# Optimization experiments

Measured on AMD Instinct MI355X. Metric: run time of the kernel, lower is better.

## Reference

```python
import jax, jax.numpy as jnp
import numpy as np

B, S, E = 4, 2048, 512
H = 8
DK = E // H          # 64
NQ = 8               # n_qubits


def setup_inputs() -> dict:
    key = jax.random.key(0)
    ks = jax.random.split(key, 10)
    s = 1.0 / np.sqrt(E)
    return {
        "x": jax.random.normal(ks[0], (B, S, E), dtype=jnp.float32),
        "Wq": jax.random.normal(ks[1], (E, E), dtype=jnp.float32) * s,
        "bq": jnp.zeros((E,), dtype=jnp.float32),
        "Wk": jax.random.normal(ks[2], (E, E), dtype=jnp.float32) * s,
        "bk": jnp.zeros((E,), dtype=jnp.float32),
        "Wv": jax.random.normal(ks[3], (E, E), dtype=jnp.float32) * s,
        "bv": jnp.zeros((E,), dtype=jnp.float32),
        "Wo": jax.random.normal(ks[4], (E, E), dtype=jnp.float32) * s,
        "bo": jnp.zeros((E,), dtype=jnp.float32),
        "kernel_params": jax.random.normal(ks[5], (NQ, NQ), dtype=jnp.float32),
    }


def _split_heads(t):
    # [B,S,E] -> [B,H,S,DK]
    return t.reshape(B, S, H, DK).transpose(0, 2, 1, 3)


def reference(x, Wq, bq, Wk, bk, Wv, bv, Wo, bo, kernel_params):
    q = _split_heads(x @ Wq + bq)
    k = _split_heads(x @ Wk + bk)
    v = _split_heads(x @ Wv + bv)

    # Quantum kernel closed form: RX(x_i) then RZ(theta_ii) on wire i, measure <Z_i>.
    # RZ commutes with Z so <Z_i> = cos(x_i). Only the first NQ features are encoded.
    q_meas = jnp.cos(q[..., :NQ])  # [B,H,S,NQ]
    k_meas = jnp.cos(k[..., :NQ])  # [B,H,S,NQ]

    sim = jnp.einsum('bhqd,bhkd->bhqk', q_meas, k_meas)  # [B,H,S,S]
    attn = jax.nn.softmax(sim, axis=-1)
    out = jnp.einsum('bhqk,bhkd->bhqd', attn, v)          # [B,H,S,DK]
    out = out.transpose(0, 2, 1, 3).reshape(B, S, E)      # compose heads
    return out @ Wo + bo
```

## Files before the change

### kernel.cpp

```cpp
#include <hip/hip_runtime.h>
#include <hip/hip_bf16.h>

#define BB 4
#define SS 2048
#define EE 512
#define HH 8
#define DKK 64
#define NQQ 8
#define BS (BB * SS)

typedef __attribute__((ext_vector_type(8))) short bf16x8;
typedef __attribute__((ext_vector_type(4))) float f32x4;
typedef __attribute__((ext_vector_type(16))) float f32x16;
typedef _Float16 f16x4 __attribute__((ext_vector_type(4)));
typedef _Float16 f16x8 __attribute__((ext_vector_type(8)));
typedef unsigned short u16;
typedef unsigned int u32;

union U2H { uint2 u; f16x4 h; };
union U4H8 { uint4 u; f16x8 h; };

__device__ __forceinline__ u16 f2bf(float f) {
    union { float f; u32 u; } v; v.f = f;
    u32 r = v.u + 0x7fffu + ((v.u >> 16) & 1u);
    return (u16)(r >> 16);
}
__device__ __forceinline__ float bf2f(u16 h) {
    union { u32 u; float f; } v; v.u = ((u32)h) << 16;
    return v.f;
}
__device__ __forceinline__ u16 f2h(float f) {
    _Float16 hv = (_Float16)f;
    return *reinterpret_cast<u16*>(&hv);
}

__global__ __launch_bounds__(256) void cvt2_kernel(
    const float4* __restrict__ in, uint2* __restrict__ xh, uint2* __restrict__ xl, int n4)
{
    int i = blockIdx.x * 256 + threadIdx.x;
    if (i >= n4) return;
    float4 a = in[i];
    u16 h0 = f2bf(a.x), h1 = f2bf(a.y), h2 = f2bf(a.z), h3 = f2bf(a.w);
    u16 l0 = f2bf(a.x - bf2f(h0)), l1 = f2bf(a.y - bf2f(h1));
    u16 l2 = f2bf(a.z - bf2f(h2)), l3 = f2bf(a.w - bf2f(h3));
    xh[i] = make_uint2((u32)h0 | ((u32)h1 << 16), (u32)h2 | ((u32)h3 << 16));
    xl[i] = make_uint2((u32)l0 | ((u32)l1 << 16), (u32)l2 | ((u32)l3 << 16));
}

__global__ __launch_bounds__(256) void wqk_pack_kernel(
    const float* __restrict__ Wq, const float* __restrict__ Wk,
    u16* __restrict__ Wh, u16* __restrict__ Wl)
{
    const int n = blockIdx.x;
    const int col = (((n & 63) >> 3) << 6) | (n & 7);
    const float* src = (n < 64) ? Wq : Wk;
    for (int k = threadIdx.x; k < EE; k += 256) {
        float v = src[(size_t)k * EE + col];
        u16 h = f2bf(v);
        Wh[(size_t)n * EE + k] = h;
        Wl[(size_t)n * EE + k] = f2bf(v - bf2f(h));
    }
}

__global__ __launch_bounds__(256) void wtrans_kernel(
    const float* __restrict__ W, u16* __restrict__ WT)
{
    __shared__ float ts[64][65];
    const int kt0 = blockIdx.x * 64, nt0 = blockIdx.y * 64;
    const int tid = threadIdx.x;
    #pragma unroll
    for (int i = 0; i < 4; ++i) {
        int c = tid + i * 256;
        int kr = c >> 4, nc = (c & 15) * 4;
        float4 t = *reinterpret_cast<const float4*>(&W[(size_t)(kt0 + kr) * EE + nt0 + nc]);
        ts[kr][nc] = t.x; ts[kr][nc + 1] = t.y; ts[kr][nc + 2] = t.z; ts[kr][nc + 3] = t.w;
    }
    __syncthreads();
    const int n = tid >> 2, k0 = (tid & 3) * 16;
    u32 o[8];
    #pragma unroll
    for (int j = 0; j < 8; ++j) {
        o[j] = (u32)f2bf(ts[k0 + 2 * j][n]) | ((u32)f2bf(ts[k0 + 2 * j + 1][n]) << 16);
    }
    uint4* dst = reinterpret_cast<uint4*>(&WT[(size_t)(nt0 + n) * EE + kt0 + k0]);
    dst[0] = make_uint4(o[0], o[1], o[2], o[3]);
    dst[1] = make_uint4(o[4], o[5], o[6], o[7]);
}

__global__ __launch_bounds__(256) void qk_mfma_kernel(
    const u16* __restrict__ xh, const u16* __restrict__ xl,
    const u16* __restrict__ Wh, const u16* __restrict__ Wl,
    const float* __restrict__ bq, const float* __restrict__ bk,
    u16* __restrict__ qf, u16* __restrict__ kf)
{
    __shared__ u16 Asl[64 * 64];
    __shared__ u16 Bsl[64 * 64];

    const int tid = threadIdx.x;
    const int lane = tid & 63;
    const int ww = tid >> 6;
    const int wr = ww >> 1, wc = ww & 1;
    const int tx = lane & 15, tyq = lane >> 4;
    const int m0 = blockIdx.x * 64;
    const int isK = blockIdx.y;
    const int nbase = isK * 64;

    const int c0 = tid, c1 = tid + 256;
    const int r0 = c0 >> 3, o0 = (c0 & 7) * 8, d0 = r0 * 64 + (((c0 & 7) ^ (r0 & 7)) * 8);
    const int r1 = c1 >> 3, o1 = (c1 & 7) * 8, d1 = r1 * 64 + (((c1 & 7) ^ (r1 & 7)) * 8);

    uint4 pa0, pa1, pb0, pb1;
    auto ldi = [&](int it) {
        int pass = it >> 3, k0 = (it & 7) * 64;
        const u16* Ab = (pass == 1) ? xl : xh;
        const u16* Bb = (pass == 2) ? Wl : Wh;
        pa0 = *reinterpret_cast<const uint4*>(&Ab[(size_t)(m0 + r0) * EE + k0 + o0]);
        pb0 = *reinterpret_cast<const uint4*>(&Bb[(size_t)(nbase + r0) * EE + k0 + o0]);
        pa1 = *reinterpret_cast<const uint4*>(&Ab[(size_t)(m0 + r1) * EE + k0 + o1]);
        pb1 = *reinterpret_cast<const uint4*>(&Bb[(size_t)(nbase + r1) * EE + k0 + o1]);
    };
    auto st = [&]() {
        *reinterpret_cast<uint4*>(&Asl[d0]) = pa0;
        *reinterpret_cast<uint4*>(&Bsl[d0]) = pb0;
        *reinterpret_cast<uint4*>(&Asl[d1]) = pa1;
        *reinterpret_cast<uint4*>(&Bsl[d1]) = pb1;
    };

    f32x4 acc[2][2];
    #pragma unroll
    for (int mt = 0; mt < 2; ++mt)
        #pragma unroll
        for (int nt = 0; nt < 2; ++nt) acc[mt][nt] = (f32x4)(0.f);

    const int bkx = tx & 7;
    ldi(0);
    for (int it = 0; it < 24; ++it) {
        __syncthreads();
        st();
        if (it < 23) ldi(it + 1);
        __syncthreads();
        #pragma unroll
        for (int kb = 0; kb < 2; ++kb) {
            bf16x8 af[2], bfg[2];
            const int kblk = ((kb * 4 + tyq) ^ bkx) * 8;
            #pragma unroll
            for (int mt = 0; mt < 2; ++mt)
                af[mt] = *reinterpret_cast<const bf16x8*>(&Asl[(wr * 32 + mt * 16 + tx) * 64 + kblk]);
            #pragma unroll
            for (int nt = 0; nt < 2; ++nt)
                bfg[nt] = *reinterpret_cast<const bf16x8*>(&Bsl[(wc * 32 + nt * 16 + tx) * 64 + kblk]);
            #pragma unroll
            for (int mt = 0; mt < 2; ++mt)
                #pragma unroll
                for (int nt = 0; nt < 2; ++nt)
                    acc[mt][nt] = __builtin_amdgcn_mfma_f32_16x16x32_bf16(
                        af[mt], bfg[nt], acc[mt][nt], 0, 0, 0);
        }
    }

    const float* bias = isK ? bk : bq;
    u16* dst = isK ? kf : qf;
    #pragma unroll
    for (int mt = 0; mt < 2; ++mt) {
        #pragma unroll
        for (int nt = 0; nt < 2; ++nt) {
            int nl = wc * 32 + nt * 16 + tx;
            int h = nl >> 3, f = nl & 7;
            float bcol = bias[h * 64 + f];
            #pragma unroll
            for (int r = 0; r < 4; ++r) {
                int s = m0 + wr * 32 + mt * 16 + tyq * 4 + r;
                float c = __cosf(acc[mt][nt][r] + bcol);
                size_t bh = (size_t)((s >> 11) * HH + h);
                dst[(bh * SS + (s & 2047)) * 8 + f] = f2h(c);
            }
        }
    }
}

template<int MODE>
__global__ __launch_bounds__(256) void mfma_gemm_kernel(
    const u16* __restrict__ A, const u16* __restrict__ Bm,
    const float* __restrict__ bias, float* __restrict__ outf, u16* __restrict__ outb)
{
    __shared__ u16 Asl[64 * 64];
    __shared__ u16 Bsl[64 * 64];

    const int tid = threadIdx.x;
    const int lane = tid & 63;
    const int ww = tid >> 6;
    const int wr = ww >> 1, wc = ww & 1;
    const int tx = lane & 15, tyq = lane >> 4;
    const int m0 = blockIdx.x * 64, n0 = blockIdx.y * 64;

    const int c0 = tid, c1 = tid + 256;
    const int r0 = c0 >> 3, o0 = (c0 & 7) * 8, d0 = r0 * 64 + (((c0 & 7) ^ (r0 & 7)) * 8);
    const int r1 = c1 >> 3, o1 = (c1 & 7) * 8, d1 = r1 * 64 + (((c1 & 7) ^ (r1 & 7)) * 8);

    uint4 pa0, pa1, pb0, pb1;
    auto ld = [&](int ks) {
        int k0 = ks * 64;
        pa0 = *reinterpret_cast<const uint4*>(&A [(size_t)(m0 + r0) * EE + k0 + o0]);
        pb0 = *reinterpret_cast<const uint4*>(&Bm[(size_t)(n0 + r0) * EE + k0 + o0]);
        pa1 = *reinterpret_cast<const uint4*>(&A [(size_t)(m0 + r1) * EE + k0 + o1]);
        pb1 = *reinterpret_cast<const uint4*>(&Bm[(size_t)(n0 + r1) * EE + k0 + o1]);
    };
    auto st = [&]() {
        *reinterpret_cast<uint4*>(&Asl[d0]) = pa0;
        *reinterpret_cast<uint4*>(&Bsl[d0]) = pb0;
        *reinterpret_cast<uint4*>(&Asl[d1]) = pa1;
        *reinterpret_cast<uint4*>(&Bsl[d1]) = pb1;
    };

    f32x4 acc[2][2];
    #pragma unroll
    for (int mt = 0; mt < 2; ++mt)
        #pragma unroll
        for (int nt = 0; nt < 2; ++nt) acc[mt][nt] = (f32x4)(0.f);

    const int bkx = tx & 7;
    ld(0);
    for (int ks = 0; ks < 8; ++ks) {
        __syncthreads();
        st();
        if (ks < 7) ld(ks + 1);
        __syncthreads();
        #pragma unroll
        for (int kb = 0; kb < 2; ++kb) {
            bf16x8 af[2], bfg[2];
            const int kblk = ((kb * 4 + tyq) ^ bkx) * 8;
            #pragma unroll
            for (int mt = 0; mt < 2; ++mt)
                af[mt] = *reinterpret_cast<const bf16x8*>(&Asl[(wr * 32 + mt * 16 + tx) * 64 + kblk]);
            #pragma unroll
            for (int nt = 0; nt < 2; ++nt)
                bfg[nt] = *reinterpret_cast<const bf16x8*>(&Bsl[(wc * 32 + nt * 16 + tx) * 64 + kblk]);
            #pragma unroll
            for (int mt = 0; mt < 2; ++mt)
                #pragma unroll
                for (int nt = 0; nt < 2; ++nt)
                    acc[mt][nt] = __builtin_amdgcn_mfma_f32_16x16x32_bf16(
                        af[mt], bfg[nt], acc[mt][nt], 0, 0, 0);
        }
    }

    #pragma unroll
    for (int mt = 0; mt < 2; ++mt) {
        #pragma unroll
        for (int nt = 0; nt < 2; ++nt) {
            int gcol = n0 + wc * 32 + nt * 16 + tx;
            float bcol = (MODE == 0) ? bias[gcol] : 0.f;
            #pragma unroll
            for (int r = 0; r < 4; ++r) {
                int grow = m0 + wr * 32 + mt * 16 + tyq * 4 + r;
                float v = acc[mt][nt][r];
                if (MODE == 0) {
                    outf[(size_t)grow * EE + gcol] = v + bcol;
                } else {
                    float vb = v + bias[grow];
                    size_t addr = ((size_t)((gcol >> 11) * 8 + (grow >> 6))) * (64 * 2048)
                                + (size_t)(grow & 63) * 2048 + (gcol & 2047);
                    outb[addr] = f2h(vb);
                }
            }
        }
    }
}

__global__ __launch_bounds__(256, 4) void attn_v6_kernel(
    const u16* __restrict__ qf, const u16* __restrict__ kf,
    const u16* __restrict__ VT, u16* __restrict__ attb)
{
    __shared__ u16 vtl[2][2][64 * 64];

    const int tid = threadIdx.x;
    const int lane = tid & 63;
    const int wv = tid >> 6;
    const int kslice = wv >> 1;
    const int qw = wv & 1;
    const int l31 = lane & 31;
    const int hi = lane >> 5;

    const int bid = blockIdx.x;
    const int xcd = bid & 7, sub = bid >> 3;
    const int bh = (xcd << 2) | (sub >> 5);
    const int q0 = (sub & 31) * 64;

    const u16* __restrict__ qfb = qf + (size_t)bh * SS * 8;
    const u16* __restrict__ kfb = kf + (size_t)bh * SS * 8;
    const u16* __restrict__ VTb = VT + (size_t)bh * DKK * SS;

    const uint4 z4 = make_uint4(0u, 0u, 0u, 0u);

    U4H8 qb;
    qb.u = hi ? z4 : *reinterpret_cast<const uint4*>(&qfb[(size_t)(q0 + qw * 32 + l31) * 8]);
    const f16x8 QB = qb.h;

    const int wd0 = tid >> 3, wbk = tid & 7;
    const int B0 = (wbk >> 1) * 2;
    const int offu = (wbk & 1) * 4;
    const int w0a = wd0 * 64 + ((B0 ^ (wd0 & 7)) * 8) + offu;
    const int w0b = wd0 * 64 + (((B0 + 1) ^ (wd0 & 7)) * 8) + offu;
    const int wd1 = wd0 + 32;
    const int w1a = wd1 * 64 + ((B0 ^ (wd1 & 7)) * 8) + offu;
    const int w1b = wd1 * 64 + (((B0 + 1) ^ (wd1 & 7)) * 8) + offu;

    uint4 pv[2][2];
    auto ldv = [&](int t) {
        #pragma unroll
        for (int s = 0; s < 2; ++s) {
            int kt = s * 1024 + t * 64;
            pv[s][0] = *reinterpret_cast<const uint4*>(&VTb[(size_t)wd0 * SS + kt + wbk * 8]);
            pv[s][1] = *reinterpret_cast<const uint4*>(&VTb[(size_t)wd1 * SS + kt + wbk * 8]);
        }
    };
    auto stv = [&](int buf) {
        #pragma unroll
        for (int s = 0; s < 2; ++s) {
            u16* base = &vtl[s][buf][0];
            *reinterpret_cast<uint2*>(&base[w0a]) = make_uint2(pv[s][0].x, pv[s][0].y);
            *reinterpret_cast<uint2*>(&base[w0b]) = make_uint2(pv[s][0].z, pv[s][0].w);
            *reinterpret_cast<uint2*>(&base[w1a]) = make_uint2(pv[s][1].x, pv[s][1].y);
            *reinterpret_cast<uint2*>(&base[w1b]) = make_uint2(pv[s][1].z, pv[s][1].w);
        }
    };

    f32x16 acc0 = (f32x16)(0.f), acc1 = (f32x16)(0.f);
    float z = 0.f;

    const int vr0 = l31 * 64, vr1 = (32 + l31) * 64;
    const int bx = l31 & 7;
    const int ks_off = kslice * 1024;

    U4H8 kc0, kc1, kn0, kn1;
    auto ldk = [&](int t, U4H8& a, U4H8& b) {
        int kt = ks_off + t * 64;
        a.u = hi ? z4 : *reinterpret_cast<const uint4*>(&kfb[(size_t)(kt + l31) * 8]);
        b.u = hi ? z4 : *reinterpret_cast<const uint4*>(&kfb[(size_t)(kt + 32 + l31) * 8]);
    };

    ldv(0);
    ldk(0, kc0, kc1);
    stv(0);
    __syncthreads();

    for (int t = 0; t < 16; ++t) {
        const int cur = t & 1;
        if (t < 15) { ldv(t + 1); ldk(t + 1, kn0, kn1); }

        const u16* vbase = &vtl[kslice][cur][0];
        #pragma unroll
        for (int s = 0; s < 2; ++s) {
            f32x16 sim = (f32x16)(0.f);
            sim = __builtin_amdgcn_mfma_f32_32x32x16_f16(
                s ? kc1.h : kc0.h, QB, sim, 0, 0, 0);

            float w[16];
            #pragma unroll
            for (int r = 0; r < 16; ++r) w[r] = __expf(sim[r]);
            float zp = 0.f;
            #pragma unroll
            for (int r = 0; r < 8; ++r) zp += (w[2 * r] + w[2 * r + 1]);
            z += zp;

            #pragma unroll
            for (int c = 0; c < 2; ++c) {
                f16x8 PA;
                #pragma unroll
                for (int j = 0; j < 8; ++j) PA[j] = (_Float16)w[8 * c + j];
                const int e = s * 4 + c * 2;
                f16x8 VB0 = *reinterpret_cast<const f16x8*>(&vbase[vr0 + (((e + hi) ^ bx) * 8)]);
                acc0 = __builtin_amdgcn_mfma_f32_32x32x16_f16(PA, VB0, acc0, 0, 0, 0);
                f16x8 VB1 = *reinterpret_cast<const f16x8*>(&vbase[vr1 + (((e + hi) ^ bx) * 8)]);
                acc1 = __builtin_amdgcn_mfma_f32_32x32x16_f16(PA, VB1, acc1, 0, 0, 0);
            }
        }

        if (t < 15) stv(cur ^ 1);
        __syncthreads();
        kc0 = kn0; kc1 = kn1;
    }

    float* fsh = reinterpret_cast<float*>(&vtl[0][0][0]);
    const int cbase = (qw * 64 + lane) * 33;
    if (kslice == 1) {
        #pragma unroll
        for (int r = 0; r < 16; ++r) {
            fsh[cbase + r] = acc0[r];
            fsh[cbase + 16 + r] = acc1[r];
        }
        fsh[cbase + 32] = z;
    }
    __syncthreads();
    if (kslice == 0) {
        #pragma unroll
        for (int r = 0; r < 16; ++r) {
            acc0[r] += fsh[cbase + r];
            acc1[r] += fsh[cbase + 16 + r];
        }
        z += fsh[cbase + 32];
        z += __shfl_xor(z, 32, 64);
        float zinv = 1.0f / z;

        const int b = bh >> 3, h = bh & 7;
        #pragma unroll
        for (int r = 0; r < 16; ++r) {
            int qrow = (r & 3) + 8 * (r >> 2) + 4 * hi;
            float zi = __shfl(zinv, qrow, 32);
            size_t base = ((size_t)b * SS + q0 + qw * 32 + qrow) * EE + h * DKK + l31;
            attb[base]      = f2bf(acc0[r] * zi);
            attb[base + 32] = f2bf(acc1[r] * zi);
        }
    }
}

extern "C" void kernel_launch(void* const* d_in, const int* in_sizes, int n_in,
                              void* d_out, int out_size, void* d_ws, size_t ws_size,
                              hipStream_t stream)
{
    const float* x  = (const float*)d_in[0];
    const float* Wq = (const float*)d_in[1];
    const float* bq = (const float*)d_in[2];
    const float* Wk = (const float*)d_in[3];
    const float* bk = (const float*)d_in[4];
    const float* Wv = (const float*)d_in[5];
    const float* bv = (const float*)d_in[6];
    const float* Wo = (const float*)d_in[7];
    const float* bo = (const float*)d_in[8];

    char* w = (char*)d_ws;
    u16* xh    = (u16*)w;  w += (size_t)BS * EE * 2;
    u16* xl    = (u16*)w;  w += (size_t)BS * EE * 2;
    u16* Wqkh  = (u16*)w;  w += (size_t)128 * EE * 2;
    u16* Wqkl  = (u16*)w;  w += (size_t)128 * EE * 2;
    u16* WvT   = (u16*)w;  w += (size_t)EE * EE * 2;
    u16* WoT   = (u16*)w;  w += (size_t)EE * EE * 2;
    u16* qf    = (u16*)w;  w += (size_t)BB * HH * SS * 8 * 2;
    u16* kf    = (u16*)w;  w += (size_t)BB * HH * SS * 8 * 2;
    u16* VT    = (u16*)w;  w += (size_t)BB * HH * DKK * SS * 2;
    u16* attb  = xl;
    float* out = (float*)d_out;

    cvt2_kernel<<<dim3(BS * EE / 4 / 256), 256, 0, stream>>>(
        (const float4*)x, (uint2*)xh, (uint2*)xl, BS * EE / 4);
    wqk_pack_kernel<<<dim3(128), 256, 0, stream>>>(Wq, Wk, Wqkh, Wqkl);
    wtrans_kernel<<<dim3(8, 8), 256, 0, stream>>>(Wv, WvT);
    wtrans_kernel<<<dim3(8, 8), 256, 0, stream>>>(Wo, WoT);
    qk_mfma_kernel<<<dim3(BS / 64, 2), 256, 0, stream>>>(
        xh, xl, Wqkh, Wqkl, bq, bk, qf, kf);
    mfma_gemm_kernel<1><<<dim3(EE / 64, BS / 64), 256, 0, stream>>>(
        WvT, xh, bv, nullptr, VT);
    attn_v6_kernel<<<dim3(1024), 256, 0, stream>>>(qf, kf, VT, attb);
    mfma_gemm_kernel<0><<<dim3(BS / 64, EE / 64), 256, 0, stream>>>(
        attb, WoT, bo, out, nullptr);
}
```

Measured before the change: 89.97 us.

## Switch pipeline to fp16, drop weight lo-split pass, pre-tile V for register loads

All bf16 conversions and MFMAs become fp16. The Q/K projection drops the weight low-part pass, so it runs 2 split passes instead of 3. The V projection epilogue now writes V in an MFMA-fragment-tiled layout through shared memory. The attention kernel then loads V fragments straight from global into registers, with software prefetch instead of an LDS double buffer and barriers. This trims GEMM work and removes LDS staging and syncs in attention, but fp16 has a narrower range and lower precision on the K/Q cos inputs.

```diff
diff --git a/kernel.cpp b/kernel.cpp
--- a/kernel.cpp
+++ b/kernel.cpp
@@ -9,30 +9,22 @@
 #define NQQ 8
 #define BS (BB * SS)
 
-typedef __attribute__((ext_vector_type(8))) short bf16x8;
 typedef __attribute__((ext_vector_type(4))) float f32x4;
 typedef __attribute__((ext_vector_type(16))) float f32x16;
-typedef _Float16 f16x4 __attribute__((ext_vector_type(4)));
 typedef _Float16 f16x8 __attribute__((ext_vector_type(8)));
 typedef unsigned short u16;
 typedef unsigned int u32;
 
-union U2H { uint2 u; f16x4 h; };
 union U4H8 { uint4 u; f16x8 h; };
 
-__device__ __forceinline__ u16 f2bf(float f) {
-    union { float f; u32 u; } v; v.f = f;
-    u32 r = v.u + 0x7fffu + ((v.u >> 16) & 1u);
-    return (u16)(r >> 16);
-}
-__device__ __forceinline__ float bf2f(u16 h) {
-    union { u32 u; float f; } v; v.u = ((u32)h) << 16;
-    return v.f;
-}
 __device__ __forceinline__ u16 f2h(float f) {
     _Float16 hv = (_Float16)f;
     return *reinterpret_cast<u16*>(&hv);
 }
+__device__ __forceinline__ float h2f(u16 u) {
+    _Float16 h = *reinterpret_cast<_Float16*>(&u);
+    return (float)h;
+}
 
 __global__ __launch_bounds__(256) void cvt2_kernel(
     const float4* __restrict__ in, uint2* __restrict__ xh, uint2* __restrict__ xl, int n4)
@@ -40,25 +32,22 @@
     int i = blockIdx.x * 256 + threadIdx.x;
     if (i >= n4) return;
     float4 a = in[i];
-    u16 h0 = f2bf(a.x), h1 = f2bf(a.y), h2 = f2bf(a.z), h3 = f2bf(a.w);
-    u16 l0 = f2bf(a.x - bf2f(h0)), l1 = f2bf(a.y - bf2f(h1));
-    u16 l2 = f2bf(a.z - bf2f(h2)), l3 = f2bf(a.w - bf2f(h3));
+    u16 h0 = f2h(a.x), h1 = f2h(a.y), h2 = f2h(a.z), h3 = f2h(a.w);
+    u16 l0 = f2h(a.x - h2f(h0)), l1 = f2h(a.y - h2f(h1));
+    u16 l2 = f2h(a.z - h2f(h2)), l3 = f2h(a.w - h2f(h3));
     xh[i] = make_uint2((u32)h0 | ((u32)h1 << 16), (u32)h2 | ((u32)h3 << 16));
     xl[i] = make_uint2((u32)l0 | ((u32)l1 << 16), (u32)l2 | ((u32)l3 << 16));
 }
 
 __global__ __launch_bounds__(256) void wqk_pack_kernel(
     const float* __restrict__ Wq, const float* __restrict__ Wk,
-    u16* __restrict__ Wh, u16* __restrict__ Wl)
+    u16* __restrict__ Wh)
 {
     const int n = blockIdx.x;
     const int col = (((n & 63) >> 3) << 6) | (n & 7);
     const float* src = (n < 64) ? Wq : Wk;
     for (int k = threadIdx.x; k < EE; k += 256) {
-        float v = src[(size_t)k * EE + col];
-        u16 h = f2bf(v);
-        Wh[(size_t)n * EE + k] = h;
-        Wl[(size_t)n * EE + k] = f2bf(v - bf2f(h));
+        Wh[(size_t)n * EE + k] = f2h(src[(size_t)k * EE + col]);
     }
 }
 
@@ -80,7 +69,7 @@
     u32 o[8];
     #pragma unroll
     for (int j = 0; j < 8; ++j) {
-        o[j] = (u32)f2bf(ts[k0 + 2 * j][n]) | ((u32)f2bf(ts[k0 + 2 * j + 1][n]) << 16);
+        o[j] = (u32)f2h(ts[k0 + 2 * j][n]) | ((u32)f2h(ts[k0 + 2 * j + 1][n]) << 16);
     }
     uint4* dst = reinterpret_cast<uint4*>(&WT[(size_t)(nt0 + n) * EE + kt0 + k0]);
     dst[0] = make_uint4(o[0], o[1], o[2], o[3]);
@@ -89,7 +78,7 @@
 
 __global__ __launch_bounds__(256) void qk_mfma_kernel(
     const u16* __restrict__ xh, const u16* __restrict__ xl,
-    const u16* __restrict__ Wh, const u16* __restrict__ Wl,
+    const u16* __restrict__ Wh,
     const float* __restrict__ bq, const float* __restrict__ bk,
     u16* __restrict__ qf, u16* __restrict__ kf)
 {
@@ -112,12 +101,11 @@
     uint4 pa0, pa1, pb0, pb1;
     auto ldi = [&](int it) {
         int pass = it >> 3, k0 = (it & 7) * 64;
-        const u16* Ab = (pass == 1) ? xl : xh;
-        const u16* Bb = (pass == 2) ? Wl : Wh;
+        const u16* Ab = pass ? xl : xh;
         pa0 = *reinterpret_cast<const uint4*>(&Ab[(size_t)(m0 + r0) * EE + k0 + o0]);
-        pb0 = *reinterpret_cast<const uint4*>(&Bb[(size_t)(nbase + r0) * EE + k0 + o0]);
+        pb0 = *reinterpret_cast<const uint4*>(&Wh[(size_t)(nbase + r0) * EE + k0 + o0]);
         pa1 = *reinterpret_cast<const uint4*>(&Ab[(size_t)(m0 + r1) * EE + k0 + o1]);
-        pb1 = *reinterpret_cast<const uint4*>(&Bb[(size_t)(nbase + r1) * EE + k0 + o1]);
+        pb1 = *reinterpret_cast<const uint4*>(&Wh[(size_t)(nbase + r1) * EE + k0 + o1]);
     };
     auto st = [&]() {
         *reinterpret_cast<uint4*>(&Asl[d0]) = pa0;
@@ -134,26 +122,26 @@
 
     const int bkx = tx & 7;
     ldi(0);
-    for (int it = 0; it < 24; ++it) {
+    for (int it = 0; it < 16; ++it) {
         __syncthreads();
         st();
-        if (it < 23) ldi(it + 1);
+        if (it < 15) ldi(it + 1);
         __syncthreads();
         #pragma unroll
         for (int kb = 0; kb < 2; ++kb) {
-            bf16x8 af[2], bfg[2];
+            f16x8 af[2], bfg[2];
             const int kblk = ((kb * 4 + tyq) ^ bkx) * 8;
             #pragma unroll
             for (int mt = 0; mt < 2; ++mt)
-                af[mt] = *reinterpret_cast<const bf16x8*>(&Asl[(wr * 32 + mt * 16 + tx) * 64 + kblk]);
+                af[mt] = *reinterpret_cast<const f16x8*>(&Asl[(wr * 32 + mt * 16 + tx) * 64 + kblk]);
             #pragma unroll
             for (int nt = 0; nt < 2; ++nt)
-                bfg[nt] = *reinterpret_cast<const bf16x8*>(&Bsl[(wc * 32 + nt * 16 + tx) * 64 + kblk]);
+                bfg[nt] = *reinterpret_cast<const f16x8*>(&Bsl[(wc * 32 + nt * 16 + tx) * 64 + kblk]);
             #pragma unroll
             for (int mt = 0; mt < 2; ++mt)
                 #pragma unroll
                 for (int nt = 0; nt < 2; ++nt)
-                    acc[mt][nt] = __builtin_amdgcn_mfma_f32_16x16x32_bf16(
+                    acc[mt][nt] = __builtin_amdgcn_mfma_f32_16x16x32_f16(
                         af[mt], bfg[nt], acc[mt][nt], 0, 0, 0);
         }
     }
@@ -183,8 +171,9 @@
     const u16* __restrict__ A, const u16* __restrict__ Bm,
     const float* __restrict__ bias, float* __restrict__ outf, u16* __restrict__ outb)
 {
-    __shared__ u16 Asl[64 * 64];
-    __shared__ u16 Bsl[64 * 64];
+    __shared__ u16 smem[8448];
+    u16* Asl = smem;
+    u16* Bsl = smem + 4096;
 
     const int tid = threadIdx.x;
     const int lane = tid & 63;
@@ -227,51 +216,81 @@
         __syncthreads();
         #pragma unroll
         for (int kb = 0; kb < 2; ++kb) {
-            bf16x8 af[2], bfg[2];
+            f16x8 af[2], bfg[2];
             const int kblk = ((kb * 4 + tyq) ^ bkx) * 8;
             #pragma unroll
             for (int mt = 0; mt < 2; ++mt)
-                af[mt] = *reinterpret_cast<const bf16x8*>(&Asl[(wr * 32 + mt * 16 + tx) * 64 + kblk]);
+                af[mt] = *reinterpret_cast<const f16x8*>(&Asl[(wr * 32 + mt * 16 + tx) * 64 + kblk]);
             #pragma unroll
             for (int nt = 0; nt < 2; ++nt)
-                bfg[nt] = *reinterpret_cast<const bf16x8*>(&Bsl[(wc * 32 + nt * 16 + tx) * 64 + kblk]);
+                bfg[nt] = *reinterpret_cast<const f16x8*>(&Bsl[(wc * 32 + nt * 16 + tx) * 64 + kblk]);
             #pragma unroll
             for (int mt = 0; mt < 2; ++mt)
                 #pragma unroll
                 for (int nt = 0; nt < 2; ++nt)
-                    acc[mt][nt] = __builtin_amdgcn_mfma_f32_16x16x32_bf16(
+                    acc[mt][nt] = __builtin_amdgcn_mfma_f32_16x16x32_f16(
                         af[mt], bfg[nt], acc[mt][nt], 0, 0, 0);
         }
     }
 
-    #pragma unroll
-    for (int mt = 0; mt < 2; ++mt) {
-        #pragma unroll
-        for (int nt = 0; nt < 2; ++nt) {
-            int gcol = n0 + wc * 32 + nt * 16 + tx;
-            float bcol = (MODE == 0) ? bias[gcol] : 0.f;
-            #pragma unroll
-            for (int r = 0; r < 4; ++r) {
-                int grow = m0 + wr * 32 + mt * 16 + tyq * 4 + r;
-                float v = acc[mt][nt][r];
-                if (MODE == 0) {
-                    outf[(size_t)grow * EE + gcol] = v + bcol;
-                } else {
-                    float vb = v + bias[grow];
-                    size_t addr = ((size_t)((gcol >> 11) * 8 + (grow >> 6))) * (64 * 2048)
-                                + (size_t)(grow & 63) * 2048 + (gcol & 2047);
-                    outb[addr] = f2h(vb);
+    if (MODE == 0) {
+        #pragma unroll
+        for (int mt = 0; mt < 2; ++mt) {
+            #pragma unroll
+            for (int nt = 0; nt < 2; ++nt) {
+                int gcol = n0 + wc * 32 + nt * 16 + tx;
+                float bcol = bias[gcol];
+                #pragma unroll
+                for (int r = 0; r < 4; ++r) {
+                    int grow = m0 + wr * 32 + mt * 16 + tyq * 4 + r;
+                    outf[(size_t)grow * EE + gcol] = acc[mt][nt][r] + bcol;
                 }
             }
         }
-    }
-}
-
-__global__ __launch_bounds__(256, 4) void attn_v6_kernel(
+    } else {
+        __syncthreads();
+        #pragma unroll
+        for (int mt = 0; mt < 2; ++mt) {
+            #pragma unroll
+            for (int nt = 0; nt < 2; ++nt) {
+                int kl = wc * 32 + nt * 16 + tx;
+                #pragma unroll
+                for (int r = 0; r < 4; ++r) {
+                    int dl = wr * 32 + mt * 16 + tyq * 4 + r;
+                    float vb = acc[mt][nt][r] + bias[m0 + dl];
+                    smem[dl * 66 + kl] = f2h(vb);
+                }
+            }
+        }
+        __syncthreads();
+        const size_t slab = (size_t)((n0 >> 11) * HH + (m0 >> 6)) * (SS * DKK);
+        const int cell0 = (n0 & 2047) >> 3;
+        #pragma unroll
+        for (int i = 0; i < 2; ++i) {
+            int item = tid + i * 256;
+            int d = item & 63, ci = item >> 6;
+            int kb = 16 * (ci >> 1) + 4 * (ci & 1);
+            u16 g[8];
+            #pragma unroll
+            for (int j = 0; j < 8; ++j) {
+                int klocal = kb + (j & 3) + 8 * (j >> 2);
+                g[j] = smem[d * 66 + klocal];
+            }
+            uint4 p;
+            p.x = (u32)g[0] | ((u32)g[1] << 16);
+            p.y = (u32)g[2] | ((u32)g[3] << 16);
+            p.z = (u32)g[4] | ((u32)g[5] << 16);
+            p.w = (u32)g[6] | ((u32)g[7] << 16);
+            *reinterpret_cast<uint4*>(&outb[slab + (size_t)(cell0 + ci) * 512 + d * 8]) = p;
+        }
+    }
+}
+
+__global__ __launch_bounds__(256, 4) void attn_v7_kernel(
     const u16* __restrict__ qf, const u16* __restrict__ kf,
-    const u16* __restrict__ VT, u16* __restrict__ attb)
-{
-    __shared__ u16 vtl[2][2][64 * 64];
+    const u16* __restrict__ VT2, u16* __restrict__ attb)
+{
+    __shared__ float fsh[128 * 33];
 
     const int tid = threadIdx.x;
     const int lane = tid & 63;
@@ -288,7 +307,7 @@
 
     const u16* __restrict__ qfb = qf + (size_t)bh * SS * 8;
     const u16* __restrict__ kfb = kf + (size_t)bh * SS * 8;
-    const u16* __restrict__ VTb = VT + (size_t)bh * DKK * SS;
+    const u16* __restrict__ V2b = VT2 + (size_t)bh * SS * DKK;
 
     const uint4 z4 = make_uint4(0u, 0u, 0u, 0u);
 
@@ -296,41 +315,20 @@
     qb.u = hi ? z4 : *reinterpret_cast<const uint4*>(&qfb[(size_t)(q0 + qw * 32 + l31) * 8]);
     const f16x8 QB = qb.h;
 
-    const int wd0 = tid >> 3, wbk = tid & 7;
-    const int B0 = (wbk >> 1) * 2;
-    const int offu = (wbk & 1) * 4;
-    const int w0a = wd0 * 64 + ((B0 ^ (wd0 & 7)) * 8) + offu;
-    const int w0b = wd0 * 64 + (((B0 + 1) ^ (wd0 & 7)) * 8) + offu;
-    const int wd1 = wd0 + 32;
-    const int w1a = wd1 * 64 + ((B0 ^ (wd1 & 7)) * 8) + offu;
-    const int w1b = wd1 * 64 + (((B0 + 1) ^ (wd1 & 7)) * 8) + offu;
-
-    uint4 pv[2][2];
-    auto ldv = [&](int t) {
-        #pragma unroll
-        for (int s = 0; s < 2; ++s) {
-            int kt = s * 1024 + t * 64;
-            pv[s][0] = *reinterpret_cast<const uint4*>(&VTb[(size_t)wd0 * SS + kt + wbk * 8]);
-            pv[s][1] = *reinterpret_cast<const uint4*>(&VTb[(size_t)wd1 * SS + kt + wbk * 8]);
-        }
-    };
-    auto stv = [&](int buf) {
-        #pragma unroll
-        for (int s = 0; s < 2; ++s) {
-            u16* base = &vtl[s][buf][0];
-            *reinterpret_cast<uint2*>(&base[w0a]) = make_uint2(pv[s][0].x, pv[s][0].y);
-            *reinterpret_cast<uint2*>(&base[w0b]) = make_uint2(pv[s][0].z, pv[s][0].w);
-            *reinterpret_cast<uint2*>(&base[w1a]) = make_uint2(pv[s][1].x, pv[s][1].y);
-            *reinterpret_cast<uint2*>(&base[w1b]) = make_uint2(pv[s][1].z, pv[s][1].w);
-        }
-    };
-
     f32x16 acc0 = (f32x16)(0.f), acc1 = (f32x16)(0.f);
     float z = 0.f;
 
-    const int vr0 = l31 * 64, vr1 = (32 + l31) * 64;
-    const int bx = l31 & 7;
     const int ks_off = kslice * 1024;
+
+    auto vld = [&](int t, int s, uint4* dst) {
+        const int K0 = ks_off + t * 64 + s * 32;
+        #pragma unroll
+        for (int c = 0; c < 2; ++c) {
+            const size_t cb = (size_t)((((K0 >> 4) + c) << 1) + hi) * 512;
+            dst[c * 2]     = *reinterpret_cast<const uint4*>(&V2b[cb + l31 * 8]);
+            dst[c * 2 + 1] = *reinterpret_cast<const uint4*>(&V2b[cb + (32 + l31) * 8]);
+        }
+    };
 
     U4H8 kc0, kc1, kn0, kn1;
     auto ldk = [&](int t, U4H8& a, U4H8& b) {
@@ -339,22 +337,16 @@
         b.u = hi ? z4 : *reinterpret_cast<const uint4*>(&kfb[(size_t)(kt + 32 + l31) * 8]);
     };
 
-    ldv(0);
+    uint4 vA[4], vB[4];
     ldk(0, kc0, kc1);
-    stv(0);
-    __syncthreads();
+    vld(0, 0, vA);
 
     for (int t = 0; t < 16; ++t) {
-        const int cur = t & 1;
-        if (t < 15) { ldv(t + 1); ldk(t + 1, kn0, kn1); }
-
-        const u16* vbase = &vtl[kslice][cur][0];
-        #pragma unroll
-        for (int s = 0; s < 2; ++s) {
+        vld(t, 1, vB);
+        if (t < 15) ldk(t + 1, kn0, kn1);
+        {
             f32x16 sim = (f32x16)(0.f);
-            sim = __builtin_amdgcn_mfma_f32_32x32x16_f16(
-                s ? kc1.h : kc0.h, QB, sim, 0, 0, 0);
-
+            sim = __builtin_amdgcn_mfma_f32_32x32x16_f16(kc0.h, QB, sim, 0, 0, 0);
             float w[16];
             #pragma unroll
             for (int r = 0; r < 16; ++r) w[r] = __expf(sim[r]);
@@ -362,26 +354,40 @@
             #pragma unroll
             for (int r = 0; r < 8; ++r) zp += (w[2 * r] + w[2 * r + 1]);
             z += zp;
-
             #pragma unroll
             for (int c = 0; c < 2; ++c) {
                 f16x8 PA;
                 #pragma unroll
                 for (int j = 0; j < 8; ++j) PA[j] = (_Float16)w[8 * c + j];
-                const int e = s * 4 + c * 2;
-                f16x8 VB0 = *reinterpret_cast<const f16x8*>(&vbase[vr0 + (((e + hi) ^ bx) * 8)]);
-                acc0 = __builtin_amdgcn_mfma_f32_32x32x16_f16(PA, VB0, acc0, 0, 0, 0);
-                f16x8 VB1 = *reinterpret_cast<const f16x8*>(&vbase[vr1 + (((e + hi) ^ bx) * 8)]);
-                acc1 = __builtin_amdgcn_mfma_f32_32x32x16_f16(PA, VB1, acc1, 0, 0, 0);
-            }
-        }
-
-        if (t < 15) stv(cur ^ 1);
-        __syncthreads();
+                U4H8 b0, b1; b0.u = vA[c * 2]; b1.u = vA[c * 2 + 1];
+                acc0 = __builtin_amdgcn_mfma_f32_32x32x16_f16(PA, b0.h, acc0, 0, 0, 0);
+                acc1 = __builtin_amdgcn_mfma_f32_32x32x16_f16(PA, b1.h, acc1, 0, 0, 0);
+            }
+        }
+        if (t < 15) vld(t + 1, 0, vA);
+        {
+            f32x16 sim = (f32x16)(0.f);
+            sim = __builtin_amdgcn_mfma_f32_32x32x16_f16(kc1.h, QB, sim, 0, 0, 0);
+            float w[16];
+            #pragma unroll
+            for (int r = 0; r < 16; ++r) w[r] = __expf(sim[r]);
+            float zp = 0.f;
+            #pragma unroll
+            for (int r = 0; r < 8; ++r) zp += (w[2 * r] + w[2 * r + 1]);
+            z += zp;
+            #pragma unroll
+            for (int c = 0; c < 2; ++c) {
+                f16x8 PA;
+                #pragma unroll
+                for (int j = 0; j < 8; ++j) PA[j] = (_Float16)w[8 * c + j];
+                U4H8 b0, b1; b0.u = vB[c * 2]; b1.u = vB[c * 2 + 1];
+                acc0 = __builtin_amdgcn_mfma_f32_32x32x16_f16(PA, b0.h, acc0, 0, 0, 0);
+                acc1 = __builtin_amdgcn_mfma_f32_32x32x16_f16(PA, b1.h, acc1, 0, 0, 0);
+            }
+        }
         kc0 = kn0; kc1 = kn1;
     }
 
-    float* fsh = reinterpret_cast<float*>(&vtl[0][0][0]);
     const int cbase = (qw * 64 + lane) * 33;
     if (kslice == 1) {
         #pragma unroll
@@ -408,8 +414,8 @@
             int qrow = (r & 3) + 8 * (r >> 2) + 4 * hi;
             float zi = __shfl(zinv, qrow, 32);
             size_t base = ((size_t)b * SS + q0 + qw * 32 + qrow) * EE + h * DKK + l31;
-            attb[base]      = f2bf(acc0[r] * zi);
-            attb[base + 32] = f2bf(acc1[r] * zi);
+            attb[base]      = f2h(acc0[r] * zi);
+            attb[base + 32] = f2h(acc1[r] * zi);
         }
     }
 }
@@ -431,26 +437,25 @@
     char* w = (char*)d_ws;
     u16* xh    = (u16*)w;  w += (size_t)BS * EE * 2;
     u16* xl    = (u16*)w;  w += (size_t)BS * EE * 2;
-    u16* Wqkh  = (u16*)w;  w += (size_t)128 * EE * 2;
-    u16* Wqkl  = (u16*)w;  w += (size_t)128 * EE * 2;
+    u16* Wqk   = (u16*)w;  w += (size_t)128 * EE * 2;
     u16* WvT   = (u16*)w;  w += (size_t)EE * EE * 2;
     u16* WoT   = (u16*)w;  w += (size_t)EE * EE * 2;
     u16* qf    = (u16*)w;  w += (size_t)BB * HH * SS * 8 * 2;
     u16* kf    = (u16*)w;  w += (size_t)BB * HH * SS * 8 * 2;
-    u16* VT    = (u16*)w;  w += (size_t)BB * HH * DKK * SS * 2;
+    u16* VT2   = (u16*)w;  w += (size_t)BB * HH * DKK * SS * 2;
     u16* attb  = xl;
     float* out = (float*)d_out;
 
     cvt2_kernel<<<dim3(BS * EE / 4 / 256), 256, 0, stream>>>(
         (const float4*)x, (uint2*)xh, (uint2*)xl, BS * EE / 4);
-    wqk_pack_kernel<<<dim3(128), 256, 0, stream>>>(Wq, Wk, Wqkh, Wqkl);
+    wqk_pack_kernel<<<dim3(128), 256, 0, stream>>>(Wq, Wk, Wqk);
     wtrans_kernel<<<dim3(8, 8), 256, 0, stream>>>(Wv, WvT);
     wtrans_kernel<<<dim3(8, 8), 256, 0, stream>>>(Wo, WoT);
     qk_mfma_kernel<<<dim3(BS / 64, 2), 256, 0, stream>>>(
-        xh, xl, Wqkh, Wqkl, bq, bk, qf, kf);
+        xh, xl, Wqk, bq, bk, qf, kf);
     mfma_gemm_kernel<1><<<dim3(EE / 64, BS / 64), 256, 0, stream>>>(
-        WvT, xh, bv, nullptr, VT);
-    attn_v6_kernel<<<dim3(1024), 256, 0, stream>>>(qf, kf, VT, attb);
+        WvT, xh, bv, nullptr, VT2);
+    attn_v7_kernel<<<dim3(1024), 256, 0, stream>>>(qf, kf, VT2, attb);
     mfma_gemm_kernel<0><<<dim3(BS / 64, EE / 64), 256, 0, stream>>>(
         attb, WoT, bo, out, nullptr);
 }
```

Measured after the change: 85.49 us. -5.0%, faster.
